# Performance work log

Hardware: AMD Instinct MI355X
Metric: run time of the kernel (lower is better)

Reference implementation:

```python
import jax, jax.numpy as jnp
import numpy as np

PAD = -10000.0
B, N, F = 512, 2048, 16
H_PHI, LAT, H_RHO = 128, 128, 128


def _xavier(key, fan_in, fan_out):
    bound = np.sqrt(6.0 / (fan_in + fan_out))
    return jax.random.uniform(key, (fan_in, fan_out), jnp.float32, -bound, bound)


def setup_inputs() -> dict:
    key = jax.random.key(0)
    ks = jax.random.split(key, 12)
    x = jax.random.normal(ks[0], (B, N, F), jnp.float32)
    # ragged set lengths: pad tail rows with -10000.0 (the module's padding sentinel)
    lengths = jax.random.randint(ks[1], (B,), 1, N + 1)
    pad_mask = jnp.arange(N)[None, :] >= lengths[:, None]  # True where padded
    x = jnp.where(pad_mask[:, :, None], PAD, x)
    params = {
        "phi_w0": _xavier(ks[2], F, H_PHI), "phi_b0": jnp.zeros((H_PHI,), jnp.float32),
        "phi_w1": _xavier(ks[3], H_PHI, H_PHI), "phi_b1": jnp.zeros((H_PHI,), jnp.float32),
        "phi_w2": _xavier(ks[4], H_PHI, H_PHI), "phi_b2": jnp.zeros((H_PHI,), jnp.float32),
        "phi_w3": _xavier(ks[5], H_PHI, LAT), "phi_b3": jnp.zeros((LAT,), jnp.float32),
        "rho_w0": _xavier(ks[6], LAT, H_RHO), "rho_b0": jnp.zeros((H_RHO,), jnp.float32),
        "rho_w1": _xavier(ks[7], H_RHO, H_RHO), "rho_b1": jnp.zeros((H_RHO,), jnp.float32),
        "rho_w2": _xavier(ks[8], H_RHO, H_RHO), "rho_b2": jnp.zeros((H_RHO,), jnp.float32),
        "rho_w3": _xavier(ks[9], H_RHO, 1), "rho_b3": jnp.zeros((1,), jnp.float32),
    }
    return {"inputs": x, **params}


def reference(inputs, phi_w0, phi_b0, phi_w1, phi_b1, phi_w2, phi_b2, phi_w3, phi_b3,
              rho_w0, rho_b0, rho_w1, rho_b1, rho_w2, rho_b2, rho_w3, rho_b3):
    b, n, f = inputs.shape
    # valid-prefix mask: sum rows before the FIRST all-(-10000) row (matches torch loop)
    is_pad = jnp.all(inputs == PAD, axis=-1)                       # [B,N]
    first = jnp.where(jnp.any(is_pad, axis=-1), jnp.argmax(is_pad, axis=-1), n)
    mask = (jnp.arange(n)[None, :] < first[:, None]).astype(inputs.dtype)  # [B,N]
    relu = jax.nn.relu
    # phi applied per point
    h = relu(inputs @ phi_w0 + phi_b0)
    h = relu(h @ phi_w1 + phi_b1)
    h = relu(h @ phi_w2 + phi_b2)
    h = relu(h @ phi_w3 + phi_b3)                                  # [B,N,LAT]
    # masked variable-length sum pooling (segment reduce)
    pooled = jnp.einsum('bnd,bn->bd', h, mask)                     # [B,LAT]
    r = relu(pooled @ rho_w0 + rho_b0)
    r = relu(r @ rho_w1 + rho_b1)
    r = relu(r @ rho_w2 + rho_b2)
    cost = (r @ rho_w3 + rho_b3)[:, 0]                             # [B]
    return cost
```

## Files before the change

kernel.cpp:

```cpp
#include <hip/hip_runtime.h>

typedef _Float16 f16;
typedef f16  f16x2  __attribute__((ext_vector_type(2)));
typedef f16  f16x8  __attribute__((ext_vector_type(8)));
typedef __fp16 h16x2 __attribute__((ext_vector_type(2)));
typedef float f32x16 __attribute__((ext_vector_type(16)));

#define B_   512
#define N_   2048
#define PADV -10000.0f

union F16x8 { f16x8 v; f16x2 h2[4]; };

__device__ __forceinline__ f16x2 pkrtz(float a, float b) {
    h16x2 r = __builtin_amdgcn_cvt_pkrtz(a, b);
    return __builtin_bit_cast(f16x2, r);
}

__global__ void prep_kernel(const float* __restrict__ w0, const float* __restrict__ w1,
                            const float* __restrict__ w2, const float* __restrict__ w3,
                            f16* __restrict__ out, float* __restrict__ pooled)
{
    int i = blockIdx.x * 256 + threadIdx.x;
    if (i < 2048) {
        out[i] = (f16)w0[(i & 15) * 128 + (i >> 4)];
    } else if (i < 51200) {
        int j = i - 2048;
        int l = j >> 14, r = j & 16383;
        int o = r >> 7, slot = r & 127;
        int s = slot >> 4, qq = (slot >> 3) & 1, jj = slot & 7;
        int sig = 32 * (s >> 1) + 16 * (s & 1) + 4 * qq + 8 * (jj >> 2) + (jj & 3);
        const float* w = (l == 0) ? w1 : (l == 1) ? w2 : w3;
        out[i] = (f16)w[sig * 128 + o];
    }
    pooled[i] = 0.f;
}

__device__ __forceinline__ int swz(int row, int chunk) {
    return row * 256 + ((chunk ^ (row & 15)) << 4);
}

__device__ __forceinline__ void gl_lds16(const void* g, void* l) {
    __builtin_amdgcn_global_load_lds(
        (const __attribute__((address_space(1))) void*)g,
        (__attribute__((address_space(3))) void*)l, 16, 0, 0);
}

__global__ __launch_bounds__(256, 3) void phi_pool_kernel(
    const float* __restrict__ x,
    const f16*  __restrict__ wtbuf,
    const float* __restrict__ pb0, const float* __restrict__ pb1,
    const float* __restrict__ pb2, const float* __restrict__ pb3,
    float* __restrict__ pooled)
{
    __shared__ f16 wS[16384];

    const int tid  = threadIdx.x;
    const int lane = tid & 63;
    const int wv   = tid >> 6;
    const int l31  = lane & 31;
    const int q    = lane >> 5;
    const int b    = blockIdx.x & 511;
    const int tile0 = (blockIdx.x >> 9) * 128;

    {
        const float4 f0 = *(const float4*)(x + ((size_t)b * N_ + tile0) * 16);
        if (f0.x == PADV && f0.y == PADV && f0.z == PADV && f0.w == PADV) return;
    }

    const int p0 = tile0 + wv * 32;

    const float* xp = x + ((size_t)b * N_ + (size_t)(p0 + l31)) * 16 + 8 * q;
    float4 a0 = ((const float4*)xp)[0];
    float4 a1 = ((const float4*)xp)[1];

    f16x8 w0f[4];
    #pragma unroll
    for (int c = 0; c < 4; ++c)
        w0f[c] = *(const f16x8*)(wtbuf + (32 * c + l31) * 16 + 8 * q);

#define STAGE(src)                                                      \
    {                                                                   \
        _Pragma("unroll")                                               \
        for (int i = 0; i < 8; ++i) {                                   \
            const int row   = wv * 32 + i * 4 + (lane >> 4);            \
            const int chunk = (lane & 15) ^ (row & 15);                 \
            const int loff  = (wv * 32 + i * 4) * 256;   \
            gl_lds16((src) + row * 128 + chunk * 8, (char*)wS + loff);  \
        }                                                               \
    }

    STAGE(wtbuf + 2048);

    bool vA = (a0.x != PADV) || (a0.y != PADV) || (a0.z != PADV) || (a0.w != PADV) ||
              (a1.x != PADV) || (a1.y != PADV) || (a1.z != PADV) || (a1.w != PADV);
    unsigned long long blA = __ballot(vA);
    const unsigned mA = (unsigned)blA | (unsigned)(blA >> 32);

    F16x8 hf[8];
    hf[0].h2[0] = pkrtz(a0.x, a0.y);
    hf[0].h2[1] = pkrtz(a0.z, a0.w);
    hf[0].h2[2] = pkrtz(a1.x, a1.y);
    hf[0].h2[3] = pkrtz(a1.z, a1.w);

    f32x16 acc[4];

    #define INIT_ACC_BIAS(pb)                                              \
        {                                                                  \
            _Pragma("unroll")                                              \
            for (int c = 0; c < 4; ++c) {                                  \
                _Pragma("unroll")                                          \
                for (int g = 0; g < 4; ++g) {                              \
                    float4 bb = *(const float4*)((pb) + 32 * c + 8 * g + 4 * q); \
                    const float* bbp = (const float*)&bb;                  \
                    _Pragma("unroll")                                      \
                    for (int e = 0; e < 4; ++e)                            \
                        acc[c][4 * g + e] = bbp[e];                        \
                }                                                          \
            }                                                              \
        }

    #define EPILOGUE()                                                     \
        {                                                                  \
            const f16x2 z2 = {(f16)0.f, (f16)0.f};                         \
            _Pragma("unroll")                                              \
            for (int s = 0; s < 8; ++s) {                                  \
                const int c = s >> 1, r0 = 8 * (s & 1);                    \
                _Pragma("unroll")                                          \
                for (int p = 0; p < 4; ++p) {                              \
                    f16x2 m = pkrtz(                                       \
                        acc[c][r0 + 2 * p], acc[c][r0 + 2 * p + 1]);       \
                    hf[s].h2[p] = __builtin_elementwise_max(m, z2);        \
                }                                                          \
            }                                                              \
        }

    INIT_ACC_BIAS(pb0);
    #pragma unroll
    for (int c = 0; c < 4; ++c)
        acc[c] = __builtin_amdgcn_mfma_f32_32x32x16_f16(w0f[c], hf[0].v, acc[c], 0, 0, 0);
    EPILOGUE();
    INIT_ACC_BIAS(pb1);

    __syncthreads();

    #pragma unroll
    for (int s = 0; s < 8; ++s) {
        f16x8 wf[4];
        #pragma unroll
        for (int c = 0; c < 4; ++c)
            wf[c] = *(const f16x8*)((const char*)wS + swz(32 * c + l31, 2 * s + q));
        #pragma unroll
        for (int c = 0; c < 4; ++c)
            acc[c] = __builtin_amdgcn_mfma_f32_32x32x16_f16(wf[c], hf[s].v, acc[c], 0, 0, 0);
    }

    __syncthreads();
    STAGE(wtbuf + 2048 + 16384);
    EPILOGUE();
    INIT_ACC_BIAS(pb2);
    __syncthreads();

    #pragma unroll
    for (int s = 0; s < 8; ++s) {
        f16x8 wf[4];
        #pragma unroll
        for (int c = 0; c < 4; ++c)
            wf[c] = *(const f16x8*)((const char*)wS + swz(32 * c + l31, 2 * s + q));
        #pragma unroll
        for (int c = 0; c < 4; ++c)
            acc[c] = __builtin_amdgcn_mfma_f32_32x32x16_f16(wf[c], hf[s].v, acc[c], 0, 0, 0);
    }

    __syncthreads();
    STAGE(wtbuf + 2048 + 32768);
    EPILOGUE();

    {
        float bL[4];
        #pragma unroll
        for (int c = 0; c < 4; ++c) bL[c] = pb3[32 * c + l31];
        #pragma unroll
        for (int c = 0; c < 4; ++c)
            #pragma unroll
            for (int r = 0; r < 16; ++r) acc[c][r] = bL[c];
    }
    __syncthreads();

    #pragma unroll
    for (int s = 0; s < 8; ++s) {
        f16x8 wf[4];
        #pragma unroll
        for (int c = 0; c < 4; ++c)
            wf[c] = *(const f16x8*)((const char*)wS + swz(32 * c + l31, 2 * s + q));
        #pragma unroll
        for (int c = 0; c < 4; ++c)
            acc[c] = __builtin_amdgcn_mfma_f32_32x32x16_f16(hf[s].v, wf[c], acc[c], 0, 0, 0);
    }

    #pragma unroll
    for (int c = 0; c < 4; ++c) {
        float s0 = 0.f;
        #pragma unroll
        for (int r = 0; r < 16; ++r) {
            const int ptl = 4 * q + (r & 3) + 8 * (r >> 2);
            float v = fmaxf(acc[c][r], 0.f);
            s0 += ((mA >> ptl) & 1u) ? v : 0.f;
        }
        s0 += __shfl_xor(s0, 32);
        if (q == 0) atomicAdd(&pooled[b * 128 + 32 * c + l31], s0);
    }
}

__global__ __launch_bounds__(128) void rho_kernel(
    const float* __restrict__ pooled,
    const float* __restrict__ w0, const float* __restrict__ b0,
    const float* __restrict__ w1, const float* __restrict__ b1,
    const float* __restrict__ w2, const float* __restrict__ b2,
    const float* __restrict__ w3, const float* __restrict__ b3,
    float* __restrict__ out)
{
    __shared__ float buf[2][128];
    __shared__ float red[2];
    const int b = blockIdx.x, t = threadIdx.x;
    buf[0][t] = pooled[b * 128 + t];
    __syncthreads();
    const float* ws3[3] = {w0, w1, w2};
    const float* bs3[3] = {b0, b1, b2};
    int cur = 0;
    #pragma unroll 1
    for (int l = 0; l < 3; ++l) {
        float acc = bs3[l][t];
        const float* w = ws3[l];
        #pragma unroll 8
        for (int k = 0; k < 128; ++k)
            acc = fmaf(buf[cur][k], w[k * 128 + t], acc);
        buf[cur ^ 1][t] = fmaxf(acc, 0.f);
        cur ^= 1;
        __syncthreads();
    }
    float v = buf[cur][t] * w3[t];
    #pragma unroll
    for (int off = 32; off > 0; off >>= 1)
        v += __shfl_down(v, off, 64);
    if ((t & 63) == 0) red[t >> 6] = v;
    __syncthreads();
    if (t == 0) out[b] = red[0] + red[1] + b3[0];
}

extern "C" void kernel_launch(void* const* d_in, const int* in_sizes, int n_in,
                              void* d_out, int out_size, void* d_ws, size_t ws_size,
                              hipStream_t stream)
{
    (void)in_sizes; (void)n_in; (void)out_size; (void)ws_size;
    const float* x      = (const float*)d_in[0];
    const float* phi_w0 = (const float*)d_in[1];
    const float* phi_b0 = (const float*)d_in[2];
    const float* phi_w1 = (const float*)d_in[3];
    const float* phi_b1 = (const float*)d_in[4];
    const float* phi_w2 = (const float*)d_in[5];
    const float* phi_b2 = (const float*)d_in[6];
    const float* phi_w3 = (const float*)d_in[7];
    const float* phi_b3 = (const float*)d_in[8];
    const float* rho_w0 = (const float*)d_in[9];
    const float* rho_b0 = (const float*)d_in[10];
    const float* rho_w1 = (const float*)d_in[11];
    const float* rho_b1 = (const float*)d_in[12];
    const float* rho_w2 = (const float*)d_in[13];
    const float* rho_b2 = (const float*)d_in[14];
    const float* rho_w3 = (const float*)d_in[15];
    const float* rho_b3 = (const float*)d_in[16];

    float* pooled = (float*)d_ws;
    f16*   wtbuf  = (f16*)((char*)d_ws + 262144);

    prep_kernel<<<256, 256, 0, stream>>>(phi_w0, phi_w1, phi_w2, phi_w3, wtbuf, pooled);
    phi_pool_kernel<<<8192, 256, 0, stream>>>(x, wtbuf, phi_b0, phi_b1, phi_b2, phi_b3, pooled);
    rho_kernel<<<B_, 128, 0, stream>>>(pooled, rho_w0, rho_b0, rho_w1, rho_b1,
                                       rho_w2, rho_b2, rho_w3, rho_b3, (float*)d_out);
}
```

Measured before the change: 207.7 us.

## Make phi kernel persistent with all weights resident in LDS and atomic work queue

Replaces the one-block-per-tile launch with a persistent grid of 256 blocks of 12 waves. Each block loads all three 128x128 weight layers into 96KB of dynamic LDS once, and each wave then pulls 128-row tiles from one of 16 atomic counters. Within a tile, 32-row sub-tiles that are fully padded are skipped, and no barriers are needed between layers. This removes per-block weight restaging, the syncthreads between layers and launch overhead for padded tiles. The cost is counter contention, larger LDS use that limits occupancy to one block per CU, and a serial loop per wave.

```diff
diff --git a/kernel.cpp b/kernel.cpp
--- a/kernel.cpp
+++ b/kernel.cpp
@@ -19,7 +19,8 @@
 
 __global__ void prep_kernel(const float* __restrict__ w0, const float* __restrict__ w1,
                             const float* __restrict__ w2, const float* __restrict__ w3,
-                            f16* __restrict__ out, float* __restrict__ pooled)
+                            f16* __restrict__ out, float* __restrict__ pooled,
+                            unsigned* __restrict__ cnt)
 {
     int i = blockIdx.x * 256 + threadIdx.x;
     if (i < 2048) {
@@ -34,6 +35,7 @@
         out[i] = (f16)w[sig * 128 + o];
     }
     pooled[i] = 0.f;
+    if (blockIdx.x == 255 && threadIdx.x < 16) cnt[threadIdx.x] = 0u;
 }
 
 __device__ __forceinline__ int swz(int row, int chunk) {
@@ -46,64 +48,38 @@
         (__attribute__((address_space(3))) void*)l, 16, 0, 0);
 }
 
-__global__ __launch_bounds__(256, 3) void phi_pool_kernel(
+__global__ __launch_bounds__(768, 3) void phi_pool_kernel(
     const float* __restrict__ x,
     const f16*  __restrict__ wtbuf,
     const float* __restrict__ pb0, const float* __restrict__ pb1,
     const float* __restrict__ pb2, const float* __restrict__ pb3,
-    float* __restrict__ pooled)
+    float* __restrict__ pooled, unsigned* __restrict__ cnt)
 {
-    __shared__ f16 wS[16384];
+    extern __shared__ char smem[];
+    char* wA = smem;
+    char* wB = smem + 32768;
+    char* wC = smem + 65536;
 
     const int tid  = threadIdx.x;
     const int lane = tid & 63;
     const int wv   = tid >> 6;
     const int l31  = lane & 31;
     const int q    = lane >> 5;
-    const int b    = blockIdx.x & 511;
-    const int tile0 = (blockIdx.x >> 9) * 128;
-
-    {
-        const float4 f0 = *(const float4*)(x + ((size_t)b * N_ + tile0) * 16);
-        if (f0.x == PADV && f0.y == PADV && f0.z == PADV && f0.w == PADV) return;
-    }
-
-    const int p0 = tile0 + wv * 32;
-
-    const float* xp = x + ((size_t)b * N_ + (size_t)(p0 + l31)) * 16 + 8 * q;
-    float4 a0 = ((const float4*)xp)[0];
-    float4 a1 = ((const float4*)xp)[1];
-
-    f16x8 w0f[4];
-    #pragma unroll
-    for (int c = 0; c < 4; ++c)
-        w0f[c] = *(const f16x8*)(wtbuf + (32 * c + l31) * 16 + 8 * q);
-
-#define STAGE(src)                                                      \
-    {                                                                   \
-        _Pragma("unroll")                                               \
-        for (int i = 0; i < 8; ++i) {                                   \
-            const int row   = wv * 32 + i * 4 + (lane >> 4);            \
-            const int chunk = (lane & 15) ^ (row & 15);                 \
-            const int loff  = (wv * 32 + i * 4) * 256;   \
-            gl_lds16((src) + row * 128 + chunk * 8, (char*)wS + loff);  \
-        }                                                               \
-    }
-
-    STAGE(wtbuf + 2048);
-
-    bool vA = (a0.x != PADV) || (a0.y != PADV) || (a0.z != PADV) || (a0.w != PADV) ||
-              (a1.x != PADV) || (a1.y != PADV) || (a1.z != PADV) || (a1.w != PADV);
-    unsigned long long blA = __ballot(vA);
-    const unsigned mA = (unsigned)blA | (unsigned)(blA >> 32);
-
-    F16x8 hf[8];
-    hf[0].h2[0] = pkrtz(a0.x, a0.y);
-    hf[0].h2[1] = pkrtz(a0.z, a0.w);
-    hf[0].h2[2] = pkrtz(a1.x, a1.y);
-    hf[0].h2[3] = pkrtz(a1.z, a1.w);
-
-    f32x16 acc[4];
+
+    if (wv < 8) {
+        const f16* wsrc = wtbuf + 2048;
+        #pragma unroll
+        for (int i = 0; i < 4; ++i) {
+            const int row   = wv * 16 + i * 4 + (lane >> 4);
+            const int chunk = (lane & 15) ^ (row & 15);
+            const int loff  = (wv * 16 + i * 4) * 256;
+            gl_lds16(wsrc +         row * 128 + chunk * 8, wA + loff);
+            gl_lds16(wsrc + 16384 + row * 128 + chunk * 8, wB + loff);
+            gl_lds16(wsrc + 32768 + row * 128 + chunk * 8, wC + loff);
+        }
+    }
+
+    __syncthreads();
 
     #define INIT_ACC_BIAS(pb)                                              \
         {                                                                  \
@@ -128,87 +104,139 @@
                 const int c = s >> 1, r0 = 8 * (s & 1);                    \
                 _Pragma("unroll")                                          \
                 for (int p = 0; p < 4; ++p) {                              \
-                    f16x2 m = pkrtz(                                       \
+                    f16x2 mm = pkrtz(                                      \
                         acc[c][r0 + 2 * p], acc[c][r0 + 2 * p + 1]);       \
-                    hf[s].h2[p] = __builtin_elementwise_max(m, z2);        \
+                    hf[s].h2[p] = __builtin_elementwise_max(mm, z2);       \
                 }                                                          \
             }                                                              \
         }
 
-    INIT_ACC_BIAS(pb0);
-    #pragma unroll
-    for (int c = 0; c < 4; ++c)
-        acc[c] = __builtin_amdgcn_mfma_f32_32x32x16_f16(w0f[c], hf[0].v, acc[c], 0, 0, 0);
-    EPILOGUE();
-    INIT_ACC_BIAS(pb1);
-
-    __syncthreads();
-
-    #pragma unroll
-    for (int s = 0; s < 8; ++s) {
-        f16x8 wf[4];
-        #pragma unroll
-        for (int c = 0; c < 4; ++c)
-            wf[c] = *(const f16x8*)((const char*)wS + swz(32 * c + l31, 2 * s + q));
-        #pragma unroll
-        for (int c = 0; c < 4; ++c)
-            acc[c] = __builtin_amdgcn_mfma_f32_32x32x16_f16(wf[c], hf[s].v, acc[c], 0, 0, 0);
-    }
-
-    __syncthreads();
-    STAGE(wtbuf + 2048 + 16384);
-    EPILOGUE();
-    INIT_ACC_BIAS(pb2);
-    __syncthreads();
-
-    #pragma unroll
-    for (int s = 0; s < 8; ++s) {
-        f16x8 wf[4];
-        #pragma unroll
-        for (int c = 0; c < 4; ++c)
-            wf[c] = *(const f16x8*)((const char*)wS + swz(32 * c + l31, 2 * s + q));
-        #pragma unroll
-        for (int c = 0; c < 4; ++c)
-            acc[c] = __builtin_amdgcn_mfma_f32_32x32x16_f16(wf[c], hf[s].v, acc[c], 0, 0, 0);
-    }
-
-    __syncthreads();
-    STAGE(wtbuf + 2048 + 32768);
-    EPILOGUE();
-
+    const int slot = (blockIdx.x + wv) & 15;
+    unsigned* cp = cnt + slot;
+
+    unsigned m;
     {
-        float bL[4];
-        #pragma unroll
-        for (int c = 0; c < 4; ++c) bL[c] = pb3[32 * c + l31];
-        #pragma unroll
-        for (int c = 0; c < 4; ++c)
-            #pragma unroll
-            for (int r = 0; r < 16; ++r) acc[c][r] = bL[c];
-    }
-    __syncthreads();
-
-    #pragma unroll
-    for (int s = 0; s < 8; ++s) {
-        f16x8 wf[4];
-        #pragma unroll
-        for (int c = 0; c < 4; ++c)
-            wf[c] = *(const f16x8*)((const char*)wS + swz(32 * c + l31, 2 * s + q));
-        #pragma unroll
-        for (int c = 0; c < 4; ++c)
-            acc[c] = __builtin_amdgcn_mfma_f32_32x32x16_f16(hf[s].v, wf[c], acc[c], 0, 0, 0);
-    }
-
-    #pragma unroll
-    for (int c = 0; c < 4; ++c) {
-        float s0 = 0.f;
-        #pragma unroll
-        for (int r = 0; r < 16; ++r) {
-            const int ptl = 4 * q + (r & 3) + 8 * (r >> 2);
-            float v = fmaxf(acc[c][r], 0.f);
-            s0 += ((mA >> ptl) & 1u) ? v : 0.f;
-        }
-        s0 += __shfl_xor(s0, 32);
-        if (q == 0) atomicAdd(&pooled[b * 128 + 32 * c + l31], s0);
+        unsigned mn = 0;
+        if (lane == 0) mn = atomicAdd(cp, 1u);
+        m = (unsigned)__builtin_amdgcn_readfirstlane((int)mn);
+    }
+
+    #pragma unroll 1
+    for (;;) {
+        if (m >= 512u) break;
+        const int b      = slot * 32 + (int)(m & 31);
+        const int p0base = (int)(m >> 5) << 7;
+        const float* xb  = x + ((size_t)b * N_ + p0base) * 16;
+
+        unsigned mn = 0;
+        if (lane == 0) mn = atomicAdd(cp, 1u);
+
+        int pvm;
+        {
+            const float4 q0 = *(const float4*)(xb);
+            const float4 q1 = *(const float4*)(xb + 32 * 16);
+            const float4 q2 = *(const float4*)(xb + 64 * 16);
+            const float4 q3 = *(const float4*)(xb + 96 * 16);
+            const int v0 = !(q0.x == PADV && q0.y == PADV && q0.z == PADV && q0.w == PADV);
+            const int v1 = !(q1.x == PADV && q1.y == PADV && q1.z == PADV && q1.w == PADV);
+            const int v2 = !(q2.x == PADV && q2.y == PADV && q2.z == PADV && q2.w == PADV);
+            const int v3 = !(q3.x == PADV && q3.y == PADV && q3.z == PADV && q3.w == PADV);
+            pvm = v0 | (v1 << 1) | (v2 << 2) | (v3 << 3);
+        }
+
+        #pragma unroll 1
+        for (int j = 0; j < 4; ++j) {
+            if (!((pvm >> j) & 1)) continue;
+
+            const float* xp = xb + (size_t)(j * 32 + l31) * 16 + 8 * q;
+            float4 a0 = ((const float4*)xp)[0];
+            float4 a1 = ((const float4*)xp)[1];
+
+            f16x8 w0f[4];
+            #pragma unroll
+            for (int c = 0; c < 4; ++c)
+                w0f[c] = *(const f16x8*)(wtbuf + (32 * c + l31) * 16 + 8 * q);
+
+            bool vA = (a0.x != PADV) || (a0.y != PADV) || (a0.z != PADV) || (a0.w != PADV) ||
+                      (a1.x != PADV) || (a1.y != PADV) || (a1.z != PADV) || (a1.w != PADV);
+            unsigned long long blA = __ballot(vA);
+            const unsigned mskA = (unsigned)blA | (unsigned)(blA >> 32);
+
+            F16x8 hf[8];
+            hf[0].h2[0] = pkrtz(a0.x, a0.y);
+            hf[0].h2[1] = pkrtz(a0.z, a0.w);
+            hf[0].h2[2] = pkrtz(a1.x, a1.y);
+            hf[0].h2[3] = pkrtz(a1.z, a1.w);
+
+            f32x16 acc[4];
+
+            INIT_ACC_BIAS(pb0);
+            #pragma unroll
+            for (int c = 0; c < 4; ++c)
+                acc[c] = __builtin_amdgcn_mfma_f32_32x32x16_f16(w0f[c], hf[0].v, acc[c], 0, 0, 0);
+            EPILOGUE();
+
+            INIT_ACC_BIAS(pb1);
+            #pragma unroll
+            for (int s = 0; s < 8; ++s) {
+                f16x8 wf[4];
+                #pragma unroll
+                for (int c = 0; c < 4; ++c)
+                    wf[c] = *(const f16x8*)(wA + swz(32 * c + l31, 2 * s + q));
+                #pragma unroll
+                for (int c = 0; c < 4; ++c)
+                    acc[c] = __builtin_amdgcn_mfma_f32_32x32x16_f16(wf[c], hf[s].v, acc[c], 0, 0, 0);
+            }
+            EPILOGUE();
+
+            INIT_ACC_BIAS(pb2);
+            #pragma unroll
+            for (int s = 0; s < 8; ++s) {
+                f16x8 wf[4];
+                #pragma unroll
+                for (int c = 0; c < 4; ++c)
+                    wf[c] = *(const f16x8*)(wB + swz(32 * c + l31, 2 * s + q));
+                #pragma unroll
+                for (int c = 0; c < 4; ++c)
+                    acc[c] = __builtin_amdgcn_mfma_f32_32x32x16_f16(wf[c], hf[s].v, acc[c], 0, 0, 0);
+            }
+            EPILOGUE();
+
+            {
+                float bl3[4];
+                #pragma unroll
+                for (int c = 0; c < 4; ++c) bl3[c] = pb3[32 * c + l31];
+                #pragma unroll
+                for (int c = 0; c < 4; ++c)
+                    #pragma unroll
+                    for (int r = 0; r < 16; ++r) acc[c][r] = bl3[c];
+            }
+            #pragma unroll
+            for (int s = 0; s < 8; ++s) {
+                f16x8 wf[4];
+                #pragma unroll
+                for (int c = 0; c < 4; ++c)
+                    wf[c] = *(const f16x8*)(wC + swz(32 * c + l31, 2 * s + q));
+                #pragma unroll
+                for (int c = 0; c < 4; ++c)
+                    acc[c] = __builtin_amdgcn_mfma_f32_32x32x16_f16(hf[s].v, wf[c], acc[c], 0, 0, 0);
+            }
+
+            #pragma unroll
+            for (int c = 0; c < 4; ++c) {
+                float s0 = 0.f;
+                #pragma unroll
+                for (int r = 0; r < 16; ++r) {
+                    const int ptl = 4 * q + (r & 3) + 8 * (r >> 2);
+                    float v = fmaxf(acc[c][r], 0.f);
+                    s0 += ((mskA >> ptl) & 1u) ? v : 0.f;
+                }
+                s0 += __shfl_xor(s0, 32);
+                if (q == 0) atomicAdd(&pooled[b * 128 + 32 * c + l31], s0);
+            }
+        }
+
+        m = (unsigned)__builtin_amdgcn_readfirstlane((int)mn);
     }
 }
 
@@ -271,11 +299,20 @@
     const float* rho_w3 = (const float*)d_in[15];
     const float* rho_b3 = (const float*)d_in[16];
 
-    float* pooled = (float*)d_ws;
-    f16*   wtbuf  = (f16*)((char*)d_ws + 262144);
-
-    prep_kernel<<<256, 256, 0, stream>>>(phi_w0, phi_w1, phi_w2, phi_w3, wtbuf, pooled);
-    phi_pool_kernel<<<8192, 256, 0, stream>>>(x, wtbuf, phi_b0, phi_b1, phi_b2, phi_b3, pooled);
+    float*    pooled = (float*)d_ws;
+    f16*      wtbuf  = (f16*)((char*)d_ws + 262144);
+    unsigned* cnt    = (unsigned*)((char*)d_ws + 364544);
+
+    static int smem_set = 0;
+    if (!smem_set) {
+        hipFuncSetAttribute((const void*)phi_pool_kernel,
+                            hipFuncAttributeMaxDynamicSharedMemorySize, 98304);
+        smem_set = 1;
+    }
+
+    prep_kernel<<<256, 256, 0, stream>>>(phi_w0, phi_w1, phi_w2, phi_w3, wtbuf, pooled, cnt);
+    phi_pool_kernel<<<256, 768, 98304, stream>>>(x, wtbuf, phi_b0, phi_b1, phi_b2, phi_b3,
+                                                 pooled, cnt);
     rho_kernel<<<B_, 128, 0, stream>>>(pooled, rho_w0, rho_b0, rho_w1, rho_b1,
                                        rho_w2, rho_b2, rho_w3, rho_b3, (float*)d_out);
 }
```

After: 286.8 us. 38.1% more time.
